# Performance work log

Hardware: AMD Instinct MI355X
Metric: run time of the kernel (lower is better)

The kernel has to match this reference:

```python
import jax, jax.numpy as jnp
import numpy as np

N = 100000   # nodes
E = 625000   # edges
H = 128      # hidden dim
G = 64       # graphs in batch
HOPS = 5
EPS = 1e-5


def _gelu(x):
    return jax.nn.gelu(x, approximate=False)  # torch nn.GELU default (exact erf)


def _bn(x, g, b):
    # BatchNorm1d in training mode: batch statistics, biased variance
    m = jnp.mean(x, axis=0)
    v = jnp.var(x, axis=0)
    return (x - m) * jax.lax.rsqrt(v + EPS) * g + b


def _ffnn(x, W1, b1, W2, b2):
    # Linear -> GELU -> Linear -> GELU
    return _gelu(_gelu(x @ W1 + b1) @ W2 + b2)


def _vn_mlp(x, W1, b1, g1, be1, W2, b2, g2, be2):
    # Linear -> BN -> GELU -> Linear -> BN -> GELU
    h = _gelu(_bn(x @ W1 + b1, g1, be1))
    return _gelu(_bn(h @ W2 + b2, g2, be2))


def _gcn(x, W, b, src, dst):
    # PyG GCNConv: xW, symmetric-normalized aggregation over edges w/ self loops, + bias
    h = x @ W
    deg = jax.ops.segment_sum(jnp.ones_like(src, dtype=h.dtype), dst, num_segments=N)
    dinv = jax.lax.rsqrt(jnp.maximum(deg, 1.0))  # deg >= 1 due to self loops
    norm = dinv[src] * dinv[dst]                 # [E+N]
    out = jax.ops.segment_sum(h[src] * norm[:, None], dst, num_segments=N)
    return out + b


def _forward(x, edge_index, batch, pre_W1, pre_b1, pre_W2, pre_b2, conv_W, conv_b,
             bn_g, bn_b, ffn_W1, ffn_b1, ffn_W2, ffn_b2, vn_W1, vn_b1, vn_g1, vn_be1,
             vn_W2, vn_b2, vn_g2, vn_be2, vn_emb, post_W1, post_b1, post_W2, post_b2):
    loop = jnp.arange(N)
    src = jnp.concatenate([edge_index[0], loop])
    dst = jnp.concatenate([edge_index[1], loop])

    x = _ffnn(x.astype(jnp.float32), pre_W1, pre_b1, pre_W2, pre_b2)
    vn = jnp.broadcast_to(vn_emb[0], (G, H))  # vn(zeros(num_graphs))

    counts = jax.ops.segment_sum(jnp.ones((N,), x.dtype), batch, num_segments=G)
    inv_counts = 1.0 / jnp.maximum(counts, 1.0)

    for i in range(HOPS):
        x = x + vn[batch]
        x = _gcn(x, conv_W[i], conv_b[i], src, dst) + x
        x = _bn(x, bn_g[i], bn_b[i])
        x = _ffnn(x, ffn_W1[i], ffn_b1[i], ffn_W2[i], ffn_b2[i]) + x
        # dropout p=0.0 -> identity
        if i < HOPS - 1:
            pooled = jax.ops.segment_sum(x, batch, num_segments=G) * inv_counts[:, None]
            vn = vn + pooled
            vn = _vn_mlp(vn, vn_W1[i], vn_b1[i], vn_g1[i], vn_be1[i],
                         vn_W2[i], vn_b2[i], vn_g2[i], vn_be2[i])

    x = jax.ops.segment_sum(x, batch, num_segments=G)  # global_add_pool
    return _ffnn(x, post_W1, post_b1, post_W2, post_b2)


def setup_inputs():
    key = jax.random.key(0)
    ks = iter(jax.random.split(key, 40))
    def nrm(shape, s=0.05):
        return jax.random.normal(next(ks), shape, dtype=jnp.float32) * s
    d = {}
    d["x"] = jax.random.normal(next(ks), (N, H), dtype=jnp.float32)
    d["edge_index"] = jax.random.randint(next(ks), (2, E), 0, N)
    d["batch"] = jnp.sort(jax.random.randint(next(ks), (N,), 0, G))
    d["pre_W1"] = nrm((H, 2 * H)); d["pre_b1"] = jnp.zeros((2 * H,), jnp.float32)
    d["pre_W2"] = nrm((2 * H, H)); d["pre_b2"] = jnp.zeros((H,), jnp.float32)
    d["conv_W"] = nrm((HOPS, H, H)); d["conv_b"] = jnp.zeros((HOPS, H), jnp.float32)
    d["bn_g"] = jnp.ones((HOPS, H), jnp.float32); d["bn_b"] = jnp.zeros((HOPS, H), jnp.float32)
    d["ffn_W1"] = nrm((HOPS, H, 2 * H)); d["ffn_b1"] = jnp.zeros((HOPS, 2 * H), jnp.float32)
    d["ffn_W2"] = nrm((HOPS, 2 * H, H)); d["ffn_b2"] = jnp.zeros((HOPS, H), jnp.float32)
    d["vn_W1"] = nrm((HOPS - 1, H, 2 * H)); d["vn_b1"] = jnp.zeros((HOPS - 1, 2 * H), jnp.float32)
    d["vn_g1"] = jnp.ones((HOPS - 1, 2 * H), jnp.float32); d["vn_be1"] = jnp.zeros((HOPS - 1, 2 * H), jnp.float32)
    d["vn_W2"] = nrm((HOPS - 1, 2 * H, H)); d["vn_b2"] = jnp.zeros((HOPS - 1, H), jnp.float32)
    d["vn_g2"] = jnp.ones((HOPS - 1, H), jnp.float32); d["vn_be2"] = jnp.zeros((HOPS - 1, H), jnp.float32)
    d["vn_emb"] = nrm((1, H))
    d["post_W1"] = nrm((H, 2 * H)); d["post_b1"] = jnp.zeros((2 * H,), jnp.float32)
    d["post_W2"] = nrm((2 * H, H)); d["post_b2"] = jnp.zeros((H,), jnp.float32)
    return d


def reference(x, edge_index, batch, pre_W1, pre_b1, pre_W2, pre_b2, conv_W, conv_b,
              bn_g, bn_b, ffn_W1, ffn_b1, ffn_W2, ffn_b2, vn_W1, vn_b1, vn_g1, vn_be1,
              vn_W2, vn_b2, vn_g2, vn_be2, vn_emb, post_W1, post_b1, post_W2, post_b2):
    return _forward(x, edge_index, batch, pre_W1, pre_b1, pre_W2, pre_b2, conv_W, conv_b,
                    bn_g, bn_b, ffn_W1, ffn_b1, ffn_W2, ffn_b2, vn_W1, vn_b1, vn_g1, vn_be1,
                    vn_W2, vn_b2, vn_g2, vn_be2, vn_emb, post_W1, post_b1, post_W2, post_b2)
```

## Files before the change

### kernel.cpp

```cpp
#include <hip/hip_runtime.h>
#include <math.h>

#define H 128
#define H2 256
#define LDK 72
#define LDH 264
#define LDC 136
#define FFN_SMEM (64 * LDH + H * LDK)

typedef __attribute__((ext_vector_type(8))) short short8;
typedef __attribute__((ext_vector_type(4))) float floatx4;

__device__ __forceinline__ float gelu_f(float x) {
  return 0.5f * x * (1.0f + erff(x * 0.70710678118654752440f));
}

__device__ __forceinline__ unsigned short f2b(float f) {
  union { float f; unsigned u; } c; c.f = f;
  unsigned r = c.u + 0x7fffu + ((c.u >> 16) & 1u);
  return (unsigned short)(r >> 16);
}

__device__ __forceinline__ float b2f(unsigned short u) {
  union { unsigned u; float f; } c; c.u = ((unsigned)u) << 16; return c.f;
}

__device__ __forceinline__ short8 pack8(floatx4 a, floatx4 b) {
  union { short8 v; unsigned short s[8]; } u;
  u.s[0] = f2b(a.x); u.s[1] = f2b(a.y); u.s[2] = f2b(a.z); u.s[3] = f2b(a.w);
  u.s[4] = f2b(b.x); u.s[5] = f2b(b.y); u.s[6] = f2b(b.z); u.s[7] = f2b(b.w);
  return u.v;
}

__global__ __launch_bounds__(256) void transpose_w(const float* __restrict__ W, unsigned short* __restrict__ WT,
                                                   int K, int Ncol, int total) {
  int i = blockIdx.x * 256 + threadIdx.x;
  if (i >= total) return;
  int kn = K * Ncol;
  int b = i / kn, r = i - b * kn;
  int k = r / Ncol, n = r - k * Ncol;
  WT[b * kn + n * K + k] = f2b(W[i]);
}


__global__ __launch_bounds__(256) void hist_kernel(int* __restrict__ cnt, const int* __restrict__ dst, int E) {
  int i = blockIdx.x * 256 + threadIdx.x;
  if (i < E) atomicAdd(&cnt[dst[i]], 1);
}

__global__ __launch_bounds__(256) void scan_a(const int* __restrict__ cnt, int* __restrict__ row_ptr,
                                              int* __restrict__ blockSum, float* __restrict__ dinv, int N) {
  __shared__ int ls[256];
  int t = threadIdx.x;
  int idx = blockIdx.x * 1024 + t * 4;
  int4 v = make_int4(0, 0, 0, 0);
  if (idx + 3 < N) v = *(const int4*)&cnt[idx];
  else {
    if (idx + 0 < N) v.x = cnt[idx + 0];
    if (idx + 1 < N) v.y = cnt[idx + 1];
    if (idx + 2 < N) v.z = cnt[idx + 2];
    if (idx + 3 < N) v.w = cnt[idx + 3];
  }
  if (idx + 0 < N) dinv[idx + 0] = rsqrtf((float)v.x + 1.0f);
  if (idx + 1 < N) dinv[idx + 1] = rsqrtf((float)v.y + 1.0f);
  if (idx + 2 < N) dinv[idx + 2] = rsqrtf((float)v.z + 1.0f);
  if (idx + 3 < N) dinv[idx + 3] = rsqrtf((float)v.w + 1.0f);
  int s = v.x + v.y + v.z + v.w;
  ls[t] = s;
  __syncthreads();
  for (int off = 1; off < 256; off <<= 1) {
    int a = (t >= off) ? ls[t - off] : 0;
    __syncthreads();
    ls[t] += a;
    __syncthreads();
  }
  int p = ls[t] - s;
  if (t == 255) blockSum[blockIdx.x] = ls[255];
  if (idx + 0 < N) row_ptr[idx + 0] = p;  p += v.x;
  if (idx + 1 < N) row_ptr[idx + 1] = p;  p += v.y;
  if (idx + 2 < N) row_ptr[idx + 2] = p;  p += v.z;
  if (idx + 3 < N) row_ptr[idx + 3] = p;
}

__global__ __launch_bounds__(1024) void scan_b(const int* __restrict__ blockSum, int* __restrict__ blockOff,
                                               int nb, int* __restrict__ row_ptr, int N, int E) {
  __shared__ int ls[1024];
  int t = threadIdx.x;
  int s = (t < nb) ? blockSum[t] : 0;
  ls[t] = s;
  __syncthreads();
  for (int off = 1; off < 1024; off <<= 1) {
    int a = (t >= off) ? ls[t - off] : 0;
    __syncthreads();
    ls[t] += a;
    __syncthreads();
  }
  if (t < nb) blockOff[t] = ls[t] - s;
  if (t == 0) row_ptr[N] = E;
}

__global__ __launch_bounds__(256) void scan_c(int* __restrict__ row_ptr, const int* __restrict__ blockOff, int N) {
  int t = threadIdx.x;
  int idx = blockIdx.x * 1024 + t * 4;
  int off = blockOff[blockIdx.x];
  if (off == 0) return;
  if (idx + 3 < N) {
    int4 v = *(const int4*)&row_ptr[idx];
    v.x += off; v.y += off; v.z += off; v.w += off;
    *(int4*)&row_ptr[idx] = v;
  } else {
    if (idx + 0 < N) row_ptr[idx + 0] += off;
    if (idx + 1 < N) row_ptr[idx + 1] += off;
    if (idx + 2 < N) row_ptr[idx + 2] += off;
    if (idx + 3 < N) row_ptr[idx + 3] += off;
  }
}

__global__ __launch_bounds__(256) void build_csr_kernel(const int* __restrict__ src, const int* __restrict__ dst,
                                                        const int* __restrict__ row_ptr, int* __restrict__ cursor,
                                                        const float* __restrict__ dinv,
                                                        int* __restrict__ csr_src, float* __restrict__ csr_norm,
                                                        int E) {
  int i = blockIdx.x * 256 + threadIdx.x;
  if (i < E) {
    int s = src[i], d = dst[i];
    int pos = row_ptr[d] + atomicAdd(&cursor[d], 1);
    csr_src[pos] = s;
    csr_norm[pos] = dinv[s] * dinv[d];
  }
}


__global__ __launch_bounds__(256) void count_kernel(float* counts, const int* __restrict__ batch, int N, int G) {
  __shared__ float hist[256];
  int t = threadIdx.x;
  if (t < G) hist[t] = 0.f;
  __syncthreads();
  int i0 = (blockIdx.x * 256 + t) * 16;
  int cur = -1; float run = 0.f;
  for (int j = 0; j < 16; j++) {
    int i = i0 + j;
    if (i < N) {
      int b = batch[i];
      if (b == cur) run += 1.f;
      else { if (cur >= 0) atomicAdd(&hist[cur], run); cur = b; run = 1.f; }
    }
  }
  if (cur >= 0) atomicAdd(&hist[cur], run);
  __syncthreads();
  if (t < G && hist[t] != 0.f) atomicAdd(&counts[t], hist[t]);
}

__global__ __launch_bounds__(256) void vn_init_kernel(float* vn, const float* __restrict__ emb, int n) {
  int i = blockIdx.x * 256 + threadIdx.x;
  if (i < n) vn[i] = emb[i & (H - 1)];
}

__global__ __launch_bounds__(256) void gather_agg(const unsigned short* __restrict__ h, const int* __restrict__ csr_src,
                                                  const float* __restrict__ csr_norm, const int* __restrict__ row_ptr,
                                                  const float* __restrict__ dinv, const float* __restrict__ vn,
                                                  const int* __restrict__ batch, const float* __restrict__ bias,
                                                  float* __restrict__ x, int N) {
  int node = blockIdx.x * 4 + (threadIdx.x >> 6);
  if (node >= N) return;
  int lane = threadIdx.x & 63;
  int c = lane * 2;
  float di = dinv[node];
  unsigned hv = *(const unsigned*)&h[(long)node * H + c];
  float ax = b2f((unsigned short)hv) * di * di;
  float ay = b2f((unsigned short)(hv >> 16)) * di * di;
  int beg = row_ptr[node], end = row_ptr[node + 1];
  int e = beg;
  for (; e + 2 <= end; e += 2) {
    int s0 = csr_src[e], s1 = csr_src[e + 1];
    float w0 = csr_norm[e], w1 = csr_norm[e + 1];
    unsigned v0 = *(const unsigned*)&h[(long)s0 * H + c];
    unsigned v1 = *(const unsigned*)&h[(long)s1 * H + c];
    ax += b2f((unsigned short)v0) * w0 + b2f((unsigned short)v1) * w1;
    ay += b2f((unsigned short)(v0 >> 16)) * w0 + b2f((unsigned short)(v1 >> 16)) * w1;
  }
  if (e < end) {
    int s0 = csr_src[e];
    float w0 = csr_norm[e];
    unsigned v0 = *(const unsigned*)&h[(long)s0 * H + c];
    ax += b2f((unsigned short)v0) * w0;
    ay += b2f((unsigned short)(v0 >> 16)) * w0;
  }
  int b = batch[node];
  float2 xo = *(const float2*)&x[(long)node * H + c];
  float2 vv = *(const float2*)&vn[b * H + c];
  float2 bi = *(const float2*)&bias[c];
  float2 r;
  r.x = ax + xo.x + vv.x + bi.x;
  r.y = ay + xo.y + vv.y + bi.y;
  *(float2*)&x[(long)node * H + c] = r;
}


__global__ __launch_bounds__(256) void bn_reduce_kernel(const float* __restrict__ x, float* __restrict__ stats, int N) {
  __shared__ float ls[256], ls2[256];
  int t = threadIdx.x;
  int c = t & (H - 1);
  int r0 = blockIdx.x * 128 + (t >> 7);
  float s = 0.f, s2 = 0.f;
  for (int k = 0; k < 64; k++) {
    int r = r0 + k * 2;
    if (r < N) { float v = x[r * H + c]; s += v; s2 += v * v; }
  }
  ls[t] = s; ls2[t] = s2;
  __syncthreads();
  if (t < 128) {
    atomicAdd(&stats[c], ls[t] + ls[t + 128]);
    atomicAdd(&stats[H + c], ls2[t] + ls2[t + 128]);
  }
}

__global__ __launch_bounds__(128) void bn_finalize_kernel(const float* __restrict__ stats, const float* __restrict__ g,
                                                          const float* __restrict__ b, float* __restrict__ scsh,
                                                          float invN) {
  int c = threadIdx.x;
  float m = stats[c] * invN;
  float v = stats[H + c] * invN - m * m;
  float sc = rsqrtf(v + 1e-5f) * g[c];
  scsh[c] = sc;
  scsh[H + c] = b[c] - m * sc;
}

__global__ __launch_bounds__(256) void pool_kernel(float* __restrict__ pooled, const float* __restrict__ x,
                                                   const int* __restrict__ batch, int N) {
  int c = threadIdx.x & 127;
  int slab = threadIdx.x >> 7;
  int r0 = blockIdx.x * 128 + slab;
  float acc = 0.f;
  int cur = -1;
  for (int k = 0; k < 64; k++) {
    int r = r0 + k * 2;
    if (r >= N) break;
    int b = batch[r];
    if (b != cur) {
      if (cur >= 0) atomicAdd(&pooled[cur * H + c], acc);
      cur = b; acc = 0.f;
    }
    acc += x[(long)r * H + c];
  }
  if (cur >= 0) atomicAdd(&pooled[cur * H + c], acc);
}

__global__ __launch_bounds__(256) void conv_gemm(const float* __restrict__ x, const unsigned short* __restrict__ BT,
                                                 const float* __restrict__ vn, const int* __restrict__ batch,
                                                 unsigned short* __restrict__ h16, int M) {
  __shared__ unsigned short Bs[H * LDC];
  int tid = threadIdx.x;
  int lane = tid & 63, w = tid >> 6;
  int row0 = blockIdx.x * 64;
  int mrow = lane & 15, quad = lane >> 4, cn = lane & 15;
  int arow = row0 + w * 16 + mrow;
  bool rin = arow < M;
  int b = rin ? batch[arow] : 0;

#pragma unroll
  for (int j = 0; j < 8; j++) {
    int chunk = j * 256 + tid;
    int n = chunk >> 4, k8 = (chunk & 15) * 8;
    *(short8*)&Bs[n * LDC + k8] = *(const short8*)&BT[(long)n * H + k8];
  }

  short8 af[4];
#pragma unroll
  for (int k0 = 0; k0 < 4; k0++) {
    int kb = k0 * 32 + quad * 8;
    floatx4 a0 = (floatx4)0.f, a1 = (floatx4)0.f;
    if (rin) {
      a0 = *(const floatx4*)&x[(long)arow * H + kb] + *(const floatx4*)&vn[b * H + kb];
      a1 = *(const floatx4*)&x[(long)arow * H + kb + 4] + *(const floatx4*)&vn[b * H + kb + 4];
    }
    af[k0] = pack8(a0, a1);
  }
  __syncthreads();

#pragma unroll
  for (int t = 0; t < 8; t++) {
    floatx4 a = (floatx4)0.f;
#pragma unroll
    for (int k0 = 0; k0 < 4; k0++) {
      int kb = k0 * 32 + quad * 8;
      short8 bf = *(const short8*)&Bs[(t * 16 + mrow) * LDC + kb];
      a = __builtin_amdgcn_mfma_f32_16x16x32_bf16(af[k0], bf, a, 0, 0, 0);
    }
    int c = t * 16 + cn;
#pragma unroll
    for (int i = 0; i < 4; i++) {
      int r = row0 + w * 16 + quad * 4 + i;
      if (r < M) h16[(long)r * H + c] = f2b(a[i]);
    }
  }
}

template <int BNRES>
__global__ __launch_bounds__(256) void ffn_fused(const float* __restrict__ A,
                                                 const unsigned short* __restrict__ W1T, const float* __restrict__ b1,
                                                 const unsigned short* __restrict__ W2T, const float* __restrict__ b2,
                                                 const float* __restrict__ scsh,
                                                 float* __restrict__ C, int M) {
  __shared__ unsigned short smem[FFN_SMEM];
  unsigned short* Bs1 = smem;
  unsigned short* Hs  = smem;
  unsigned short* Bs2 = smem + 64 * LDH;

  int tid = threadIdx.x;
  int lane = tid & 63, w = tid >> 6;
  int row0 = blockIdx.x * 64;
  int mrow = lane & 15, quad = lane >> 4, cn = lane & 15;
  int arow = row0 + w * 16 + mrow;
  bool rin = arow < M;

  short8 af[4];
#pragma unroll
  for (int k0 = 0; k0 < 4; k0++) {
    int kb = k0 * 32 + quad * 8;
    floatx4 a0 = (floatx4)0.f, a1 = (floatx4)0.f;
    if (rin) {
      a0 = *(const floatx4*)&A[(long)arow * H + kb];
      a1 = *(const floatx4*)&A[(long)arow * H + kb + 4];
      if (BNRES) {
        a0 = a0 * *(const floatx4*)&scsh[kb] + *(const floatx4*)&scsh[H + kb];
        a1 = a1 * *(const floatx4*)&scsh[kb + 4] + *(const floatx4*)&scsh[H + kb + 4];
      }
    }
    af[k0] = pack8(a0, a1);
  }

  floatx4 acc1[16];
#pragma unroll
  for (int t = 0; t < 16; t++) acc1[t] = (floatx4)0.f;

  for (int ks = 0; ks < 2; ks++) {
    if (ks > 0) __syncthreads();
#pragma unroll
    for (int j = 0; j < 8; j++) {
      int chunk = j * 256 + tid;
      int n = chunk >> 3, k8 = (chunk & 7) * 8;
      *(short8*)&Bs1[n * LDK + k8] = *(const short8*)&W1T[(long)n * H + ks * 64 + k8];
    }
    __syncthreads();
#pragma unroll
    for (int t = 0; t < 16; t++) {
      int kb = quad * 8;
      short8 bf0 = *(const short8*)&Bs1[(t * 16 + mrow) * LDK + kb];
      acc1[t] = __builtin_amdgcn_mfma_f32_16x16x32_bf16(af[ks * 2], bf0, acc1[t], 0, 0, 0);
      short8 bf1 = *(const short8*)&Bs1[(t * 16 + mrow) * LDK + 32 + kb];
      acc1[t] = __builtin_amdgcn_mfma_f32_16x16x32_bf16(af[ks * 2 + 1], bf1, acc1[t], 0, 0, 0);
    }
  }
  __syncthreads();

#pragma unroll
  for (int t = 0; t < 16; t++) {
    int c = t * 16 + cn;
    float bb = b1[c];
#pragma unroll
    for (int i = 0; i < 4; i++) {
      int r = w * 16 + quad * 4 + i;
      Hs[r * LDH + c] = f2b(gelu_f(acc1[t][i] + bb));
    }
  }
#pragma unroll
  for (int j = 0; j < 4; j++) {
    int chunk = j * 256 + tid;
    int n = chunk >> 3, k8 = (chunk & 7) * 8;
    *(short8*)&Bs2[n * LDK + k8] = *(const short8*)&W2T[(long)n * H2 + k8];
  }
  __syncthreads();

  short8 hf[8];
#pragma unroll
  for (int k0 = 0; k0 < 8; k0++)
    hf[k0] = *(const short8*)&Hs[(w * 16 + mrow) * LDH + k0 * 32 + quad * 8];

  floatx4 acc2[8];
#pragma unroll
  for (int t = 0; t < 8; t++) acc2[t] = (floatx4)0.f;

  for (int ks = 0; ks < 4; ks++) {
    if (ks > 0) {
      __syncthreads();
#pragma unroll
      for (int j = 0; j < 4; j++) {
        int chunk = j * 256 + tid;
        int n = chunk >> 3, k8 = (chunk & 7) * 8;
        *(short8*)&Bs2[n * LDK + k8] = *(const short8*)&W2T[(long)n * H2 + ks * 64 + k8];
      }
      __syncthreads();
    }
    int kk = ks * 2;
#pragma unroll
    for (int t = 0; t < 8; t++) {
      int kb0 = quad * 8;
      short8 bf0 = *(const short8*)&Bs2[(t * 16 + mrow) * LDK + kb0];
      acc2[t] = __builtin_amdgcn_mfma_f32_16x16x32_bf16(hf[kk], bf0, acc2[t], 0, 0, 0);
      short8 bf1 = *(const short8*)&Bs2[(t * 16 + mrow) * LDK + 32 + kb0];
      acc2[t] = __builtin_amdgcn_mfma_f32_16x16x32_bf16(hf[kk + 1], bf1, acc2[t], 0, 0, 0);
    }
  }

#pragma unroll
  for (int t = 0; t < 8; t++) {
    int c = t * 16 + cn;
    float bb = b2[c];
    float rsc = 0.f, rsh = 0.f;
    if (BNRES) { rsc = scsh[c]; rsh = scsh[H + c]; }
#pragma unroll
    for (int i = 0; i < 4; i++) {
      int r = row0 + w * 16 + quad * 4 + i;
      if (r < M) {
        long off = (long)r * H + c;
        float v = gelu_f(acc2[t][i] + bb);
        if (BNRES) v += C[off] * rsc + rsh;
        C[off] = v;
      }
    }
  }
}

template <int BN, int UVN>
__global__ __launch_bounds__(256) void mlp64_l1(const float* __restrict__ vn, const float* __restrict__ pooled,
                                                const float* __restrict__ counts,
                                                const float* __restrict__ W1, const float* __restrict__ b1,
                                                const float* __restrict__ g1, const float* __restrict__ be1,
                                                float* __restrict__ h1) {
  __shared__ float u[64 * H];
  __shared__ float red[8 * 64];
  int t = threadIdx.x;
  for (int idx = t; idx < 64 * H; idx += 256) {
    float v = pooled[idx];
    if (UVN) v = vn[idx] + v / fmaxf(counts[idx >> 7], 1.0f);
    u[idx] = v;
  }
  __syncthreads();
  int tc = t & 63, tg = t >> 6;
  int c = blockIdx.x * 64 + tc;
  float acc[16];
  float bj = b1[c];
#pragma unroll
  for (int g = 0; g < 16; g++) acc[g] = bj;
  for (int k0 = 0; k0 < H; k0 += 4) {
    float w0 = W1[(k0 + 0) * H2 + c];
    float w1 = W1[(k0 + 1) * H2 + c];
    float w2 = W1[(k0 + 2) * H2 + c];
    float w3 = W1[(k0 + 3) * H2 + c];
#pragma unroll
    for (int g = 0; g < 16; g++) {
      float4 v = *(const float4*)&u[(tg * 16 + g) * H + k0];
      acc[g] += v.x * w0 + v.y * w1 + v.z * w2 + v.w * w3;
    }
  }
  float sc = 1.f, sh = 0.f;
  if (BN) {
    float s = 0.f, s2 = 0.f;
#pragma unroll
    for (int g = 0; g < 16; g++) { s += acc[g]; s2 += acc[g] * acc[g]; }
    red[tg * 64 + tc] = s;
    red[256 + tg * 64 + tc] = s2;
    __syncthreads();
    float st = red[tc] + red[64 + tc] + red[128 + tc] + red[192 + tc];
    float st2 = red[256 + tc] + red[320 + tc] + red[384 + tc] + red[448 + tc];
    float m = st * (1.f / 64.f);
    float var = st2 * (1.f / 64.f) - m * m;
    sc = rsqrtf(var + 1e-5f) * g1[c];
    sh = be1[c] - m * sc;
  }
#pragma unroll
  for (int g = 0; g < 16; g++) h1[(tg * 16 + g) * H2 + c] = gelu_f(acc[g] * sc + sh);
}

template <int BN>
__global__ __launch_bounds__(256) void mlp64_l2(const float* __restrict__ h1,
                                                const float* __restrict__ W2, const float* __restrict__ b2,
                                                const float* __restrict__ g2, const float* __restrict__ be2,
                                                float* __restrict__ outp) {
  __shared__ float red[8 * 64];
  int t = threadIdx.x;
  int tc = t & 63, tg = t >> 6;
  int c = blockIdx.x * 64 + tc;
  float acc[16];
  float bj = b2[c];
#pragma unroll
  for (int g = 0; g < 16; g++) acc[g] = bj;
  for (int k0 = 0; k0 < H2; k0 += 4) {
    float w0 = W2[(k0 + 0) * H + c];
    float w1 = W2[(k0 + 1) * H + c];
    float w2 = W2[(k0 + 2) * H + c];
    float w3 = W2[(k0 + 3) * H + c];
#pragma unroll
    for (int g = 0; g < 16; g++) {
      float4 v = *(const float4*)&h1[(tg * 16 + g) * H2 + k0];
      acc[g] += v.x * w0 + v.y * w1 + v.z * w2 + v.w * w3;
    }
  }
  float sc = 1.f, sh = 0.f;
  if (BN) {
    float s = 0.f, s2 = 0.f;
#pragma unroll
    for (int g = 0; g < 16; g++) { s += acc[g]; s2 += acc[g] * acc[g]; }
    red[tg * 64 + tc] = s;
    red[256 + tg * 64 + tc] = s2;
    __syncthreads();
    float st = red[tc] + red[64 + tc] + red[128 + tc] + red[192 + tc];
    float st2 = red[256 + tc] + red[320 + tc] + red[384 + tc] + red[448 + tc];
    float m = st * (1.f / 64.f);
    float var = st2 * (1.f / 64.f) - m * m;
    sc = rsqrtf(var + 1e-5f) * g2[c];
    sh = be2[c] - m * sc;
  }
#pragma unroll
  for (int g = 0; g < 16; g++) outp[(tg * 16 + g) * H + c] = gelu_f(acc[g] * sc + sh);
}


extern "C" void kernel_launch(void* const* d_in, const int* in_sizes, int n_in,
                              void* d_out, int out_size, void* d_ws, size_t ws_size,
                              hipStream_t stream) {
  const float* x_in   = (const float*)d_in[0];
  const int*   edge   = (const int*)d_in[1];
  const int*   batch  = (const int*)d_in[2];
  const float* pre_W1 = (const float*)d_in[3];
  const float* pre_b1 = (const float*)d_in[4];
  const float* pre_W2 = (const float*)d_in[5];
  const float* pre_b2 = (const float*)d_in[6];
  const float* conv_W = (const float*)d_in[7];
  const float* conv_b = (const float*)d_in[8];
  const float* bn_g   = (const float*)d_in[9];
  const float* bn_b   = (const float*)d_in[10];
  const float* ffn_W1 = (const float*)d_in[11];
  const float* ffn_b1 = (const float*)d_in[12];
  const float* ffn_W2 = (const float*)d_in[13];
  const float* ffn_b2 = (const float*)d_in[14];
  const float* vn_W1  = (const float*)d_in[15];
  const float* vn_b1  = (const float*)d_in[16];
  const float* vn_g1  = (const float*)d_in[17];
  const float* vn_be1 = (const float*)d_in[18];
  const float* vn_W2  = (const float*)d_in[19];
  const float* vn_b2  = (const float*)d_in[20];
  const float* vn_g2  = (const float*)d_in[21];
  const float* vn_be2 = (const float*)d_in[22];
  const float* vn_emb = (const float*)d_in[23];
  const float* post_W1= (const float*)d_in[24];
  const float* post_b1= (const float*)d_in[25];
  const float* post_W2= (const float*)d_in[26];
  const float* post_b2= (const float*)d_in[27];
  float* out = (float*)d_out;

  const int N    = in_sizes[2];
  const int E    = in_sizes[1] / 2;
  const int G    = out_size / H;
  const int HOPS = in_sizes[7] / (H * H);
  const int NH   = N * H;

  float* w = (float*)d_ws;
  float* buf_x  = w;  w += NH;
  float* buf_t  = w;  w += N * H2;
  unsigned short* buf_h16 = (unsigned short*)buf_t;
  float* dinv   = w;  w += N;
  float* counts = w;  w += G;
  float* stats  = w;  w += 2 * H;
  float* scsh   = w;  w += 2 * H;
  float* pooled = w;  w += G * H;
  float* vn     = w;  w += G * H;
  float* mlp_h1 = w;  w += G * H2;
  float* csr_norm = w; w += E;
  int* iw = (int*)w;
  int* cnt      = iw;  iw += N;
  int* row_ptr  = iw;  iw += N + 1;
  int* cursor   = iw;  iw += N;
  int* csr_src  = iw;  iw += E;
  int* blockSum = iw;  iw += 1024;
  int* blockOff = iw;  iw += 1024;
  unsigned short* wt = (unsigned short*)iw;
  unsigned short* preW1T = wt;  wt += H * H2;
  unsigned short* preW2T = wt;  wt += H2 * H;
  unsigned short* convT  = wt;  wt += HOPS * H * H;
  unsigned short* ffn1T  = wt;  wt += HOPS * H * H2;
  unsigned short* ffn2T  = wt;  wt += HOPS * H2 * H;

  const int* src = edge;
  const int* dst = edge + E;

  int gE  = (E + 255) / 256;
  int gM  = (N + 63) / 64;
  int nb  = (N + 1023) / 1024;

  transpose_w<<<(H * H2 + 255) / 256, 256, 0, stream>>>(pre_W1, preW1T, H, H2, H * H2);
  transpose_w<<<(H2 * H + 255) / 256, 256, 0, stream>>>(pre_W2, preW2T, H2, H, H2 * H);
  transpose_w<<<(HOPS * H * H + 255) / 256, 256, 0, stream>>>(conv_W, convT, H, H, HOPS * H * H);
  transpose_w<<<(HOPS * H * H2 + 255) / 256, 256, 0, stream>>>(ffn_W1, ffn1T, H, H2, HOPS * H * H2);
  transpose_w<<<(HOPS * H2 * H + 255) / 256, 256, 0, stream>>>(ffn_W2, ffn2T, H2, H, HOPS * H2 * H);

  hipMemsetAsync(cnt, 0, N * sizeof(int), stream);
  hist_kernel<<<gE, 256, 0, stream>>>(cnt, dst, E);
  scan_a<<<nb, 256, 0, stream>>>(cnt, row_ptr, blockSum, dinv, N);
  scan_b<<<1, 1024, 0, stream>>>(blockSum, blockOff, nb, row_ptr, N, E);
  scan_c<<<nb, 256, 0, stream>>>(row_ptr, blockOff, N);
  hipMemsetAsync(cursor, 0, N * sizeof(int), stream);
  build_csr_kernel<<<gE, 256, 0, stream>>>(src, dst, row_ptr, cursor, dinv, csr_src, csr_norm, E);

  hipMemsetAsync(counts, 0, G * sizeof(float), stream);
  count_kernel<<<(N + 256 * 16 - 1) / (256 * 16), 256, 0, stream>>>(counts, batch, N, G);
  vn_init_kernel<<<(G * H + 255) / 256, 256, 0, stream>>>(vn, vn_emb, G * H);

  ffn_fused<0><<<gM, 256, 0, stream>>>(x_in, preW1T, pre_b1, preW2T, pre_b2, nullptr, buf_x, N);

  for (int i = 0; i < HOPS; i++) {
    conv_gemm<<<gM, 256, 0, stream>>>(buf_x, convT + i * H * H, vn, batch, buf_h16, N);
    gather_agg<<<(N + 3) / 4, 256, 0, stream>>>(buf_h16, csr_src, csr_norm, row_ptr, dinv, vn, batch, conv_b + i * H, buf_x, N);
    hipMemsetAsync(stats, 0, 2 * H * sizeof(float), stream);
    bn_reduce_kernel<<<(N + 127) / 128, 256, 0, stream>>>(buf_x, stats, N);
    bn_finalize_kernel<<<1, 128, 0, stream>>>(stats, bn_g + i * H, bn_b + i * H, scsh, 1.0f / (float)N);
    ffn_fused<1><<<gM, 256, 0, stream>>>(buf_x, ffn1T + i * H * H2, ffn_b1 + i * H2,
                                         ffn2T + i * H2 * H, ffn_b2 + i * H, scsh, buf_x, N);
    if (i < HOPS - 1) {
      hipMemsetAsync(pooled, 0, G * H * sizeof(float), stream);
      pool_kernel<<<(N + 127) / 128, 256, 0, stream>>>(pooled, buf_x, batch, N);
      mlp64_l1<1, 1><<<H2 / 64, 256, 0, stream>>>(vn, pooled, counts,
                                                  vn_W1 + i * H * H2, vn_b1 + i * H2, vn_g1 + i * H2, vn_be1 + i * H2,
                                                  mlp_h1);
      mlp64_l2<1><<<H / 64, 256, 0, stream>>>(mlp_h1, vn_W2 + i * H2 * H, vn_b2 + i * H, vn_g2 + i * H, vn_be2 + i * H, vn);
    }
  }

  hipMemsetAsync(pooled, 0, G * H * sizeof(float), stream);
  pool_kernel<<<(N + 127) / 128, 256, 0, stream>>>(pooled, buf_x, batch, N);
  mlp64_l1<0, 0><<<H2 / 64, 256, 0, stream>>>(nullptr, pooled, nullptr, post_W1, post_b1, nullptr, nullptr, mlp_h1);
  mlp64_l2<0><<<H / 64, 256, 0, stream>>>(mlp_h1, post_W2, post_b2, nullptr, nullptr, out);
}
```

Measured before the change: 2.016 ms.

## Fuse BN statistics into aggregation and pooling into FFN epilogue

The GCN gather kernel now handles 8 nodes per wave and accumulates per-channel sum and sum of squares. It reduces them in shared memory and atomically adds them to the BN stats, which replaces the separate bn_reduce pass over x. The BN finalize step moves into the FFN kernel prologue. The FFN epilogue also accumulates per-graph pooled sums, using shared-memory atomics for nearby graph ids and global atomics otherwise, which removes the pool_kernel read of x. This saves two full passes over the node features per hop plus several launches, at the cost of many atomics in the FFN epilogue.

```diff
diff --git a/kernel.cpp b/kernel.cpp
--- a/kernel.cpp
+++ b/kernel.cpp
@@ -160,90 +160,59 @@
                                                   const float* __restrict__ csr_norm, const int* __restrict__ row_ptr,
                                                   const float* __restrict__ dinv, const float* __restrict__ vn,
                                                   const int* __restrict__ batch, const float* __restrict__ bias,
-                                                  float* __restrict__ x, int N) {
-  int node = blockIdx.x * 4 + (threadIdx.x >> 6);
-  if (node >= N) return;
-  int lane = threadIdx.x & 63;
+                                                  float* __restrict__ x, float* __restrict__ stats, int N) {
+  __shared__ float sred[4 * H];
+  __shared__ float qred[4 * H];
+  int w = threadIdx.x >> 6, lane = threadIdx.x & 63;
   int c = lane * 2;
-  float di = dinv[node];
-  unsigned hv = *(const unsigned*)&h[(long)node * H + c];
-  float ax = b2f((unsigned short)hv) * di * di;
-  float ay = b2f((unsigned short)(hv >> 16)) * di * di;
-  int beg = row_ptr[node], end = row_ptr[node + 1];
-  int e = beg;
-  for (; e + 2 <= end; e += 2) {
-    int s0 = csr_src[e], s1 = csr_src[e + 1];
-    float w0 = csr_norm[e], w1 = csr_norm[e + 1];
-    unsigned v0 = *(const unsigned*)&h[(long)s0 * H + c];
-    unsigned v1 = *(const unsigned*)&h[(long)s1 * H + c];
-    ax += b2f((unsigned short)v0) * w0 + b2f((unsigned short)v1) * w1;
-    ay += b2f((unsigned short)(v0 >> 16)) * w0 + b2f((unsigned short)(v1 >> 16)) * w1;
-  }
-  if (e < end) {
-    int s0 = csr_src[e];
-    float w0 = csr_norm[e];
-    unsigned v0 = *(const unsigned*)&h[(long)s0 * H + c];
-    ax += b2f((unsigned short)v0) * w0;
-    ay += b2f((unsigned short)(v0 >> 16)) * w0;
-  }
-  int b = batch[node];
-  float2 xo = *(const float2*)&x[(long)node * H + c];
-  float2 vv = *(const float2*)&vn[b * H + c];
   float2 bi = *(const float2*)&bias[c];
-  float2 r;
-  r.x = ax + xo.x + vv.x + bi.x;
-  r.y = ay + xo.y + vv.y + bi.y;
-  *(float2*)&x[(long)node * H + c] = r;
-}
-
-
-__global__ __launch_bounds__(256) void bn_reduce_kernel(const float* __restrict__ x, float* __restrict__ stats, int N) {
-  __shared__ float ls[256], ls2[256];
+  float s0 = 0.f, s1 = 0.f, q0 = 0.f, q1 = 0.f;
+  int base = blockIdx.x * 32 + w * 8;
+  for (int j = 0; j < 8; j++) {
+    int node = base + j;
+    if (node >= N) break;
+    float di = dinv[node];
+    unsigned hv = *(const unsigned*)&h[(long)node * H + c];
+    float ax = b2f((unsigned short)hv) * di * di;
+    float ay = b2f((unsigned short)(hv >> 16)) * di * di;
+    int beg = row_ptr[node], end = row_ptr[node + 1];
+    int e = beg;
+    for (; e + 2 <= end; e += 2) {
+      int sa = csr_src[e], sb = csr_src[e + 1];
+      float w0 = csr_norm[e], w1 = csr_norm[e + 1];
+      unsigned v0 = *(const unsigned*)&h[(long)sa * H + c];
+      unsigned v1 = *(const unsigned*)&h[(long)sb * H + c];
+      ax += b2f((unsigned short)v0) * w0 + b2f((unsigned short)v1) * w1;
+      ay += b2f((unsigned short)(v0 >> 16)) * w0 + b2f((unsigned short)(v1 >> 16)) * w1;
+    }
+    if (e < end) {
+      int sa = csr_src[e];
+      float w0 = csr_norm[e];
+      unsigned v0 = *(const unsigned*)&h[(long)sa * H + c];
+      ax += b2f((unsigned short)v0) * w0;
+      ay += b2f((unsigned short)(v0 >> 16)) * w0;
+    }
+    int b = batch[node];
+    float2 xo = *(const float2*)&x[(long)node * H + c];
+    float2 vv = *(const float2*)&vn[b * H + c];
+    float rx = ax + xo.x + vv.x + bi.x;
+    float ry = ay + xo.y + vv.y + bi.y;
+    *(float2*)&x[(long)node * H + c] = make_float2(rx, ry);
+    s0 += rx; q0 += rx * rx;
+    s1 += ry; q1 += ry * ry;
+  }
+  sred[w * H + c] = s0; sred[w * H + c + 1] = s1;
+  qred[w * H + c] = q0; qred[w * H + c + 1] = q1;
+  __syncthreads();
   int t = threadIdx.x;
-  int c = t & (H - 1);
-  int r0 = blockIdx.x * 128 + (t >> 7);
-  float s = 0.f, s2 = 0.f;
-  for (int k = 0; k < 64; k++) {
-    int r = r0 + k * 2;
-    if (r < N) { float v = x[r * H + c]; s += v; s2 += v * v; }
-  }
-  ls[t] = s; ls2[t] = s2;
-  __syncthreads();
-  if (t < 128) {
-    atomicAdd(&stats[c], ls[t] + ls[t + 128]);
-    atomicAdd(&stats[H + c], ls2[t] + ls2[t + 128]);
-  }
-}
-
-__global__ __launch_bounds__(128) void bn_finalize_kernel(const float* __restrict__ stats, const float* __restrict__ g,
-                                                          const float* __restrict__ b, float* __restrict__ scsh,
-                                                          float invN) {
-  int c = threadIdx.x;
-  float m = stats[c] * invN;
-  float v = stats[H + c] * invN - m * m;
-  float sc = rsqrtf(v + 1e-5f) * g[c];
-  scsh[c] = sc;
-  scsh[H + c] = b[c] - m * sc;
-}
-
-__global__ __launch_bounds__(256) void pool_kernel(float* __restrict__ pooled, const float* __restrict__ x,
-                                                   const int* __restrict__ batch, int N) {
-  int c = threadIdx.x & 127;
-  int slab = threadIdx.x >> 7;
-  int r0 = blockIdx.x * 128 + slab;
-  float acc = 0.f;
-  int cur = -1;
-  for (int k = 0; k < 64; k++) {
-    int r = r0 + k * 2;
-    if (r >= N) break;
-    int b = batch[r];
-    if (b != cur) {
-      if (cur >= 0) atomicAdd(&pooled[cur * H + c], acc);
-      cur = b; acc = 0.f;
-    }
-    acc += x[(long)r * H + c];
-  }
-  if (cur >= 0) atomicAdd(&pooled[cur * H + c], acc);
+  if (t < H) {
+    float s = sred[t] + sred[H + t] + sred[2 * H + t] + sred[3 * H + t];
+    if (s != 0.f) atomicAdd(&stats[t], s);
+  } else {
+    int cc = t - H;
+    float q = qred[cc] + qred[H + cc] + qred[2 * H + cc] + qred[3 * H + cc];
+    if (q != 0.f) atomicAdd(&stats[H + cc], q);
+  }
 }
 
 __global__ __launch_bounds__(256) void conv_gemm(const float* __restrict__ x, const unsigned short* __restrict__ BT,
@@ -300,9 +269,13 @@
 __global__ __launch_bounds__(256) void ffn_fused(const float* __restrict__ A,
                                                  const unsigned short* __restrict__ W1T, const float* __restrict__ b1,
                                                  const unsigned short* __restrict__ W2T, const float* __restrict__ b2,
-                                                 const float* __restrict__ scsh,
+                                                 const float* __restrict__ stats, const float* __restrict__ bn_g,
+                                                 const float* __restrict__ bn_b, float invN,
+                                                 const int* __restrict__ batch, float* __restrict__ pooled,
                                                  float* __restrict__ C, int M) {
   __shared__ unsigned short smem[FFN_SMEM];
+  __shared__ float scsh_s[2 * H];
+  __shared__ float pool_s[4 * H];
   unsigned short* Bs1 = smem;
   unsigned short* Hs  = smem;
   unsigned short* Bs2 = smem + 64 * LDH;
@@ -313,6 +286,18 @@
   int mrow = lane & 15, quad = lane >> 4, cn = lane & 15;
   int arow = row0 + w * 16 + mrow;
   bool rin = arow < M;
+
+  if (BNRES) {
+    if (tid < H) {
+      float m = stats[tid] * invN;
+      float var = stats[H + tid] * invN - m * m;
+      float sc = rsqrtf(var + 1e-5f) * bn_g[tid];
+      scsh_s[tid] = sc;
+      scsh_s[H + tid] = bn_b[tid] - m * sc;
+    }
+    for (int j = tid; j < 4 * H; j += 256) pool_s[j] = 0.f;
+    __syncthreads();
+  }
 
   short8 af[4];
 #pragma unroll
@@ -323,8 +308,8 @@
       a0 = *(const floatx4*)&A[(long)arow * H + kb];
       a1 = *(const floatx4*)&A[(long)arow * H + kb + 4];
       if (BNRES) {
-        a0 = a0 * *(const floatx4*)&scsh[kb] + *(const floatx4*)&scsh[H + kb];
-        a1 = a1 * *(const floatx4*)&scsh[kb + 4] + *(const floatx4*)&scsh[H + kb + 4];
+        a0 = a0 * *(const floatx4*)&scsh_s[kb] + *(const floatx4*)&scsh_s[H + kb];
+        a1 = a1 * *(const floatx4*)&scsh_s[kb + 4] + *(const floatx4*)&scsh_s[H + kb + 4];
       }
     }
     af[k0] = pack8(a0, a1);
@@ -403,21 +388,48 @@
     }
   }
 
+  int b0 = 0;
+  int bidx[4];
+  if (BNRES) {
+    b0 = batch[row0];
+#pragma unroll
+    for (int i = 0; i < 4; i++) {
+      int r = row0 + w * 16 + quad * 4 + i;
+      bidx[i] = (r < M) ? (batch[r] - b0) : -1;
+    }
+  }
+
 #pragma unroll
   for (int t = 0; t < 8; t++) {
     int c = t * 16 + cn;
     float bb = b2[c];
     float rsc = 0.f, rsh = 0.f;
-    if (BNRES) { rsc = scsh[c]; rsh = scsh[H + c]; }
+    if (BNRES) { rsc = scsh_s[c]; rsh = scsh_s[H + c]; }
 #pragma unroll
     for (int i = 0; i < 4; i++) {
       int r = row0 + w * 16 + quad * 4 + i;
       if (r < M) {
         long off = (long)r * H + c;
         float v = gelu_f(acc2[t][i] + bb);
-        if (BNRES) v += C[off] * rsc + rsh;
-        C[off] = v;
+        if (BNRES) {
+          v += C[off] * rsc + rsh;
+          C[off] = v;
+          if (bidx[i] >= 0) {
+            if (bidx[i] < 4) atomicAdd(&pool_s[bidx[i] * H + c], v);
+            else atomicAdd(&pooled[(long)(b0 + bidx[i]) * H + c], v);
+          }
+        } else {
+          C[off] = v;
+        }
       }
+    }
+  }
+
+  if (BNRES) {
+    __syncthreads();
+    for (int j = tid; j < 4 * H; j += 256) {
+      float pv = pool_s[j];
+      if (pv != 0.f) atomicAdd(&pooled[(long)(b0 + (j >> 7)) * H + (j & (H - 1))], pv);
     }
   }
 }
@@ -563,7 +575,6 @@
   float* dinv   = w;  w += N;
   float* counts = w;  w += G;
   float* stats  = w;  w += 2 * H;
-  float* scsh   = w;  w += 2 * H;
   float* pooled = w;  w += G * H;
   float* vn     = w;  w += G * H;
   float* mlp_h1 = w;  w += G * H2;
@@ -588,6 +599,7 @@
   int gE  = (E + 255) / 256;
   int gM  = (N + 63) / 64;
   int nb  = (N + 1023) / 1024;
+  float invN = 1.0f / (float)N;
 
   transpose_w<<<(H * H2 + 255) / 256, 256, 0, stream>>>(pre_W1, preW1T, H, H2, H * H2);
   transpose_w<<<(H2 * H + 255) / 256, 256, 0, stream>>>(pre_W2, preW2T, H2, H, H2 * H);
@@ -607,19 +619,20 @@
   count_kernel<<<(N + 256 * 16 - 1) / (256 * 16), 256, 0, stream>>>(counts, batch, N, G);
   vn_init_kernel<<<(G * H + 255) / 256, 256, 0, stream>>>(vn, vn_emb, G * H);
 
-  ffn_fused<0><<<gM, 256, 0, stream>>>(x_in, preW1T, pre_b1, preW2T, pre_b2, nullptr, buf_x, N);
+  ffn_fused<0><<<gM, 256, 0, stream>>>(x_in, preW1T, pre_b1, preW2T, pre_b2,
+                                       nullptr, nullptr, nullptr, 0.f, nullptr, nullptr, buf_x, N);
 
   for (int i = 0; i < HOPS; i++) {
     conv_gemm<<<gM, 256, 0, stream>>>(buf_x, convT + i * H * H, vn, batch, buf_h16, N);
-    gather_agg<<<(N + 3) / 4, 256, 0, stream>>>(buf_h16, csr_src, csr_norm, row_ptr, dinv, vn, batch, conv_b + i * H, buf_x, N);
     hipMemsetAsync(stats, 0, 2 * H * sizeof(float), stream);
-    bn_reduce_kernel<<<(N + 127) / 128, 256, 0, stream>>>(buf_x, stats, N);
-    bn_finalize_kernel<<<1, 128, 0, stream>>>(stats, bn_g + i * H, bn_b + i * H, scsh, 1.0f / (float)N);
+    gather_agg<<<(N + 31) / 32, 256, 0, stream>>>(buf_h16, csr_src, csr_norm, row_ptr, dinv, vn, batch,
+                                                  conv_b + i * H, buf_x, stats, N);
+    hipMemsetAsync(pooled, 0, G * H * sizeof(float), stream);
     ffn_fused<1><<<gM, 256, 0, stream>>>(buf_x, ffn1T + i * H * H2, ffn_b1 + i * H2,
-                                         ffn2T + i * H2 * H, ffn_b2 + i * H, scsh, buf_x, N);
+                                         ffn2T + i * H2 * H, ffn_b2 + i * H,
+                                         stats, bn_g + i * H, bn_b + i * H, invN,
+                                         batch, pooled, buf_x, N);
     if (i < HOPS - 1) {
-      hipMemsetAsync(pooled, 0, G * H * sizeof(float), stream);
-      pool_kernel<<<(N + 127) / 128, 256, 0, stream>>>(pooled, buf_x, batch, N);
       mlp64_l1<1, 1><<<H2 / 64, 256, 0, stream>>>(vn, pooled, counts,
                                                   vn_W1 + i * H * H2, vn_b1 + i * H2, vn_g1 + i * H2, vn_be1 + i * H2,
                                                   mlp_h1);
@@ -627,8 +640,6 @@
     }
   }
 
-  hipMemsetAsync(pooled, 0, G * H * sizeof(float), stream);
-  pool_kernel<<<(N + 127) / 128, 256, 0, stream>>>(pooled, buf_x, batch, N);
   mlp64_l1<0, 0><<<H2 / 64, 256, 0, stream>>>(nullptr, pooled, nullptr, post_W1, post_b1, nullptr, nullptr, mlp_h1);
   mlp64_l2<0><<<H / 64, 256, 0, stream>>>(mlp_h1, post_W2, post_b2, nullptr, nullptr, out);
 }
```

Result: slower. 2.119 ms (+5.1%).
